# Performance work log

Hardware: AMD Instinct MI355X
Metric: run time of the kernel (lower is better)

## Reference

```python
import jax, jax.numpy as jnp
import numpy as np

D_MODEL, D_K, D_V, N_HEADS = 1024, 64, 64, 16


def setup_inputs() -> dict:
    key = jax.random.key(0)
    ks = jax.random.split(key, 8)
    B, S = 2, 2048
    s = 0.02
    return {
        "x": jax.random.normal(ks[0], (B, S, D_MODEL), dtype=jnp.float32),
        "Wq": jax.random.normal(ks[1], (D_MODEL, N_HEADS * D_K), dtype=jnp.float32) * s,
        "bq": jnp.zeros((N_HEADS * D_K,), dtype=jnp.float32),
        "Wk": jax.random.normal(ks[2], (D_MODEL, N_HEADS * D_K), dtype=jnp.float32) * s,
        "bk": jnp.zeros((N_HEADS * D_K,), dtype=jnp.float32),
        "Wv": jax.random.normal(ks[3], (D_MODEL, N_HEADS * D_V), dtype=jnp.float32) * s,
        "bv": jnp.zeros((N_HEADS * D_V,), dtype=jnp.float32),
        "Wo": jax.random.normal(ks[4], (N_HEADS * D_V, D_MODEL), dtype=jnp.float32) * s,
    }


def reference(x, Wq, bq, Wk, bk, Wv, bv, Wo):
    B, S, _ = x.shape
    split = lambda t, d: t.reshape(B, S, N_HEADS, d).transpose(0, 2, 1, 3)  # [B,H,S,d]
    Q = split(x @ Wq + bq, D_K)
    K = split(x @ Wk + bk, D_K)
    V = split(x @ Wv + bv, D_V)
    scores = jnp.einsum("bhqd,bhkd->bhqk", Q / jnp.sqrt(jnp.float32(D_K)), K)
    # causal mask: x + (1 - 1/tril) == 0 on allowed, -inf on disallowed
    causal = jnp.tril(jnp.ones((S, S), dtype=bool))
    scores = jnp.where(causal, scores, -jnp.inf)
    attn = jax.nn.softmax(scores, axis=-1)
    out = jnp.einsum("bhqk,bhkd->bhqd", attn, V)  # [B,H,S,d_v]
    out = out.transpose(0, 2, 1, 3).reshape(B, S, N_HEADS * D_V)
    return out @ Wo
```

## Files before the change

kernel.cpp:

```cpp
#include <hip/hip_runtime.h>
#include <hip/hip_bf16.h>
#include <hip/hip_fp16.h>
#include <cstdint>

#define DEVINL __device__ __forceinline__

typedef __attribute__((ext_vector_type(4))) float floatx4;
typedef __attribute__((ext_vector_type(8))) __bf16 bf16x8;
typedef __attribute__((ext_vector_type(4))) _Float16 half4;
typedef __attribute__((ext_vector_type(8))) _Float16 half8;
typedef __attribute__((ext_vector_type(4))) unsigned short u16x4;

DEVINL floatx4 mfma_16x16x32(bf16x8 a, bf16x8 b, floatx4 c) {
  return __builtin_amdgcn_mfma_f32_16x16x32_bf16(a, b, c, 0, 0, 0);
}
DEVINL floatx4 mfma_16x16x16_f16(half4 a, half4 b, floatx4 c) {
  return __builtin_amdgcn_mfma_f32_16x16x16f16(a, b, c, 0, 0, 0);
}

DEVINL void async_copy16(const void* g, void* l) {
  __builtin_amdgcn_global_load_lds(
      (__attribute__((address_space(1))) void*)(void*)g,
      (__attribute__((address_space(3))) void*)l, 16, 0, 0);
}

#define QSCALE 0.18033688011112042f

#define VS(d, s) \
  ((d) * 128 + (((((s) >> 3)) ^ ((d) & 7)) << 4) + ((s) & 7) * 2)

__global__ void prep(const float* __restrict__ x, const float* __restrict__ Wq,
                     const float* __restrict__ Wk, const float* __restrict__ Wv,
                     const float* __restrict__ Wo,
                     __hip_bfloat16* __restrict__ xb,
                     __hip_bfloat16* __restrict__ Wt,
                     __hip_bfloat16* __restrict__ Wot) {
  const int z = blockIdx.z;
  const int tx = threadIdx.x, ty = threadIdx.y;
  if (z == 4) {
    const int bi = blockIdx.y * 32 + blockIdx.x;
    const int tid = ty * 32 + tx;
    const int base = bi * 4096 + tid * 4;
#pragma unroll
    for (int j = 0; j < 4; ++j) {
      const int i = base + j * 1024;
      const float4 v = *(const float4*)&x[i];
      u16x4 pk;
      pk[0] = __builtin_bit_cast(unsigned short, __float2bfloat16(v.x));
      pk[1] = __builtin_bit_cast(unsigned short, __float2bfloat16(v.y));
      pk[2] = __builtin_bit_cast(unsigned short, __float2bfloat16(v.z));
      pk[3] = __builtin_bit_cast(unsigned short, __float2bfloat16(v.w));
      *(u16x4*)&xb[i] = pk;
    }
    return;
  }
  __shared__ float tile[32][33];
  const float* W = (z == 0) ? Wq : (z == 1) ? Wk : (z == 2) ? Wv : Wo;
  __hip_bfloat16* dst = (z < 3) ? (Wt + ((int64_t)z << 20)) : Wot;
  const int k0 = blockIdx.x * 32, n0 = blockIdx.y * 32;
#pragma unroll
  for (int i = 0; i < 32; i += 8)
    tile[ty + i][tx] = W[(int64_t)(k0 + ty + i) * 1024 + n0 + tx];
  __syncthreads();
#pragma unroll
  for (int i = 0; i < 32; i += 8)
    dst[(int64_t)(n0 + ty + i) * 1024 + k0 + tx] =
        __float2bfloat16(tile[tx][ty + i]);
}

template <int MODE, int TM, int TN, int OCC>
__global__ __launch_bounds__(256, OCC) void gemm_bt(
    const __hip_bfloat16* __restrict__ A, const __hip_bfloat16* __restrict__ Bt,
    int M, int N, int K, const float* __restrict__ bq,
    const float* __restrict__ bk, const float* __restrict__ bv,
    __hip_bfloat16* __restrict__ Qb, __hip_bfloat16* __restrict__ Kb,
    _Float16* __restrict__ Vt, float* __restrict__ outf) {
  constexpr int MI = TM / 32, NJ = TN / 32;
  __shared__ __align__(16) char As[TM * 128];
  __shared__ __align__(16) char Bs[TN * 128];
  const int tid = threadIdx.x;
  const int wave = tid >> 6, lane = tid & 63;
  const int quad = lane >> 4, l16 = lane & 15;
  const int bm = blockIdx.x * TM, bn = blockIdx.y * TN;
  const int wm = (wave >> 1) * (TM / 2), wn = (wave & 1) * (TN / 2);
  const int sw = l16 & 7;

  floatx4 acc[MI][NJ] = {};

  for (int k0 = 0; k0 < K; k0 += 64) {
#pragma unroll
    for (int i = 0; i < TM / 32; ++i) {
      const int p = tid + i * 256;
      const int r = p >> 3, cc = (p & 7) ^ (r & 7);
      async_copy16(A + (int64_t)(bm + r) * K + k0 + cc * 8, As + p * 16);
    }
#pragma unroll
    for (int i = 0; i < TN / 32; ++i) {
      const int p = tid + i * 256;
      const int r = p >> 3, cc = (p & 7) ^ (r & 7);
      async_copy16(Bt + (int64_t)(bn + r) * K + k0 + cc * 8, Bs + p * 16);
    }
    __syncthreads();
    bf16x8 af[MI][2], bfr[NJ][2];
#pragma unroll
    for (int i = 0; i < MI; ++i)
#pragma unroll
      for (int h = 0; h < 2; ++h)
        af[i][h] = *(const bf16x8*)(As + (wm + i * 16 + l16) * 128 +
                                    (((h * 4 + quad) ^ sw) << 4));
#pragma unroll
    for (int j = 0; j < NJ; ++j)
#pragma unroll
      for (int h = 0; h < 2; ++h)
        bfr[j][h] = *(const bf16x8*)(Bs + (wn + j * 16 + l16) * 128 +
                                     (((h * 4 + quad) ^ sw) << 4));
#pragma unroll
    for (int i = 0; i < MI; ++i)
#pragma unroll
      for (int j = 0; j < NJ; ++j)
#pragma unroll
        for (int h = 0; h < 2; ++h)
          acc[i][j] = mfma_16x16x32(af[i][h], bfr[j][h], acc[i][j]);
    __syncthreads();
  }

  if (MODE == 1) {
#pragma unroll
    for (int i = 0; i < MI; ++i)
#pragma unroll
      for (int j = 0; j < NJ; ++j) {
        const int n = bn + wn + j * 16 + l16;
#pragma unroll
        for (int r = 0; r < 4; ++r) {
          const int m = bm + wm + i * 16 + quad * 4 + r;
          outf[(int64_t)m * N + n] = acc[i][j][r];
        }
      }
  } else if (bn < 2048) {
#pragma unroll
    for (int i = 0; i < MI; ++i)
#pragma unroll
      for (int j = 0; j < NJ; ++j) {
        const int n = bn + wn + j * 16 + l16;
        const int which = n >> 10, nn = n & 1023;
        const int h = nn >> 6, d = nn & 63;
        const float* bias = (which == 0) ? bq : bk;
#pragma unroll
        for (int r = 0; r < 4; ++r) {
          const int m = bm + wm + i * 16 + quad * 4 + r;
          const int b = m >> 11, s = m & 2047;
          float v = acc[i][j][r] + bias[nn];
          if (which == 0) v *= QSCALE;
          ((which == 0) ? Qb : Kb)[((int64_t)(b * 16 + h) * 2048 + s) * 64 + d] =
              __float2bfloat16(v);
        }
      }
  } else {
    char* scr = (wave & 1) ? Bs : As;
    const int h = ((bn + wn) & 1023) >> 6;
    const int bb = (bm + wm) >> 11;
    const int sbase = (bm + wm) & 2047;
    _Float16* dstV = Vt + (int64_t)(bb * 16 + h) * 64 * 2048;
#pragma unroll
    for (int phase = 0; phase < 2; ++phase) {
      __syncthreads();
      if ((wave >> 1) == phase) {
#pragma unroll
        for (int i = 0; i < 4; ++i)
#pragma unroll
          for (int j = 0; j < 4; ++j) {
            const int d = j * 16 + l16;
#pragma unroll
            for (int r = 0; r < 4; ++r) {
              const int s = i * 16 + quad * 4 + r;
              *(_Float16*)(scr + VS(d, s)) =
                  (_Float16)(acc[i][j][r] + bv[((bn + wn) & 1023) + d]);
            }
          }
      }
      __syncthreads();
      if ((wave >> 1) == phase) {
#pragma unroll
        for (int it = 0; it < 8; ++it) {
          const int idx = lane + it * 64;
          const int d = idx >> 3, sc = idx & 7;
          const half8 vv =
              *(const half8*)(scr + d * 128 + ((sc ^ (d & 7)) << 4));
          *(half8*)(dstV + (int64_t)d * 2048 + sbase + sc * 8) = vv;
        }
      }
    }
  }
}

__global__ __launch_bounds__(256, 2) void attn_kernel(
    const __hip_bfloat16* __restrict__ Qb, const __hip_bfloat16* __restrict__ Kb,
    const _Float16* __restrict__ Vt, __hip_bfloat16* __restrict__ Ab) {
  __shared__ __align__(16) char smem[32768];
  const int tid = threadIdx.x;
  const int wave = tid >> 6, lane = tid & 63;
  const int quad = lane >> 4, l16 = lane & 15;
  const int pr = (int)(blockIdx.x >> 5);
  const int bh = blockIdx.x & 31;
  const int cH = 31 - pr, cL = pr;
  const int qH = cH * 64 + wave * 16;
  const int qL = cL * 64 + wave * 16;
  const int ktmax = cH;

  const __hip_bfloat16* Qh = Qb + (int64_t)bh * 2048 * 64;
  const __hip_bfloat16* Kh = Kb + (int64_t)bh * 2048 * 64;
  const _Float16* Vh = Vt + (int64_t)bh * 64 * 2048;

  bf16x8 qfH[2], qfL[2];
#pragma unroll
  for (int h = 0; h < 2; ++h) {
    qfH[h] = *(const bf16x8*)&Qh[(int64_t)(qH + l16) * 64 + h * 32 + quad * 8];
    qfL[h] = *(const bf16x8*)&Qh[(int64_t)(qL + l16) * 64 + h * 32 + quad * 8];
  }

  floatx4 oH[4] = {}, oL[4] = {};
  float lsH = 0.f, lsL = 0.f;

  auto stage = [&](int buf, int k0s) {
#pragma unroll
    for (int i = 0; i < 2; ++i) {
      const int p = tid + i * 256;
      const int r = p >> 3, cc = (p & 7) ^ (r & 7);
      async_copy16(Kh + (int64_t)(k0s + r) * 64 + cc * 8,
                   smem + buf * 8192 + p * 16);
      async_copy16(Vh + (int64_t)r * 2048 + k0s + cc * 8,
                   smem + 16384 + buf * 8192 + p * 16);
    }
  };

  stage(0, 0);
  for (int kt = 0; kt <= ktmax; ++kt) {
    const int k0 = kt * 64;
    const int cur = kt & 1;
    __syncthreads();
    if (kt < ktmax) stage(cur ^ 1, k0 + 64);

    const char* kb = smem + cur * 8192;
    const char* vb = smem + 16384 + cur * 8192;
    const int sw = l16 & 7;
    const bool doL = (kt <= cL);

    bf16x8 kfr[4][2];
#pragma unroll
    for (int kk = 0; kk < 4; ++kk)
#pragma unroll
      for (int h = 0; h < 2; ++h)
        kfr[kk][h] = *(const bf16x8*)(kb + (kk * 16 + l16) * 128 +
                                      (((h * 4 + quad) ^ sw) << 4));
    half4 vfr[4][4];
#pragma unroll
    for (int dt = 0; dt < 4; ++dt)
#pragma unroll
      for (int kk = 0; kk < 4; ++kk)
        vfr[dt][kk] = *(const half4*)(vb + (dt * 16 + l16) * 128 +
                                      (((kk * 2 + (quad >> 1)) ^ sw) << 4) +
                                      (quad & 1) * 8);

    floatx4 stH[4], stL[4];
    __builtin_amdgcn_s_setprio(1);
#pragma unroll
    for (int kk = 0; kk < 4; ++kk) {
      floatx4 z = {};
      z = mfma_16x16x32(kfr[kk][0], qfH[0], z);
      stH[kk] = mfma_16x16x32(kfr[kk][1], qfH[1], z);
    }
    if (doL) {
#pragma unroll
      for (int kk = 0; kk < 4; ++kk) {
        floatx4 z = {};
        z = mfma_16x16x32(kfr[kk][0], qfL[0], z);
        stL[kk] = mfma_16x16x32(kfr[kk][1], qfL[1], z);
      }
    }
    __builtin_amdgcn_s_setprio(0);

    {
      const bool masked = (kt == cH);
      half4 pf[4];
#pragma unroll
      for (int kk = 0; kk < 4; ++kk) {
#pragma unroll
        for (int r = 0; r < 4; ++r) {
          const int key = k0 + kk * 16 + quad * 4 + r;
          float p = __builtin_amdgcn_exp2f(stH[kk][r]);
          if (masked && key > qH + l16) p = 0.f;
          lsH += p;
          pf[kk][r] = (_Float16)p;
        }
      }
      __builtin_amdgcn_s_setprio(1);
#pragma unroll
      for (int dt = 0; dt < 4; ++dt)
#pragma unroll
        for (int kk = 0; kk < 4; ++kk)
          oH[dt] = mfma_16x16x16_f16(vfr[dt][kk], pf[kk], oH[dt]);
      __builtin_amdgcn_s_setprio(0);
    }
    if (doL) {
      const bool masked = (kt == cL);
      half4 pf[4];
#pragma unroll
      for (int kk = 0; kk < 4; ++kk) {
#pragma unroll
        for (int r = 0; r < 4; ++r) {
          const int key = k0 + kk * 16 + quad * 4 + r;
          float p = __builtin_amdgcn_exp2f(stL[kk][r]);
          if (masked && key > qL + l16) p = 0.f;
          lsL += p;
          pf[kk][r] = (_Float16)p;
        }
      }
      __builtin_amdgcn_s_setprio(1);
#pragma unroll
      for (int dt = 0; dt < 4; ++dt)
#pragma unroll
        for (int kk = 0; kk < 4; ++kk)
          oL[dt] = mfma_16x16x16_f16(vfr[dt][kk], pf[kk], oL[dt]);
      __builtin_amdgcn_s_setprio(0);
    }
  }

  lsH += __shfl_xor(lsH, 16, 64);
  lsH += __shfl_xor(lsH, 32, 64);
  lsL += __shfl_xor(lsL, 16, 64);
  lsL += __shfl_xor(lsL, 32, 64);
  const float invH = 1.0f / lsH;
  const float invL = 1.0f / lsL;

  const int b = bh >> 4, h = bh & 15;
#pragma unroll
  for (int dt = 0; dt < 4; ++dt) {
    u16x4 packH, packL;
#pragma unroll
    for (int r = 0; r < 4; ++r) {
      packH[r] = __builtin_bit_cast(unsigned short,
                                    __float2bfloat16(oH[dt][r] * invH));
      packL[r] = __builtin_bit_cast(unsigned short,
                                    __float2bfloat16(oL[dt][r] * invL));
    }
    *(u16x4*)&Ab[(int64_t)(b * 2048 + qH + l16) * 1024 + h * 64 + dt * 16 +
                 quad * 4] = packH;
    *(u16x4*)&Ab[(int64_t)(b * 2048 + qL + l16) * 1024 + h * 64 + dt * 16 +
                 quad * 4] = packL;
  }
}

extern "C" void kernel_launch(void* const* d_in, const int* in_sizes, int n_in,
                              void* d_out, int out_size, void* d_ws,
                              size_t ws_size, hipStream_t stream) {
  const float* x = (const float*)d_in[0];
  const float* Wq = (const float*)d_in[1];
  const float* bq = (const float*)d_in[2];
  const float* Wk = (const float*)d_in[3];
  const float* bk = (const float*)d_in[4];
  const float* Wv = (const float*)d_in[5];
  const float* bv = (const float*)d_in[6];
  const float* Wo = (const float*)d_in[7];
  float* out = (float*)d_out;

  char* ws = (char*)d_ws;
  __hip_bfloat16* xb = (__hip_bfloat16*)(ws);
  __hip_bfloat16* Wt = (__hip_bfloat16*)(ws + (8ll << 20));
  __hip_bfloat16* Wot = (__hip_bfloat16*)(ws + (14ll << 20));
  __hip_bfloat16* Qb = (__hip_bfloat16*)(ws + (16ll << 20));
  __hip_bfloat16* Kb = (__hip_bfloat16*)(ws + (24ll << 20));
  _Float16* Vt = (_Float16*)(ws + (32ll << 20));
  __hip_bfloat16* Ab = xb;

  prep<<<dim3(32, 32, 5), dim3(32, 8), 0, stream>>>(x, Wq, Wk, Wv, Wo, xb, Wt,
                                                    Wot);
  gemm_bt<0, 128, 128, 3><<<dim3(32, 24), 256, 0, stream>>>(
      xb, Wt, 4096, 3072, 1024, bq, bk, bv, Qb, Kb, Vt, nullptr);
  attn_kernel<<<dim3(512), 256, 0, stream>>>(Qb, Kb, Vt, Ab);
  gemm_bt<1, 128, 64, 2><<<dim3(32, 16), 256, 0, stream>>>(
      Ab, Wot, 4096, 1024, 1024, nullptr, nullptr, nullptr, nullptr, nullptr,
      nullptr, out);
}
```

Baseline: 165.5 us.

## Add dedicated 256x256 double-buffered QKV projection GEMM kernel

Result: slower. 172.3 us (+4.1%).

```diff
diff --git a/kernel.cpp b/kernel.cpp
--- a/kernel.cpp
+++ b/kernel.cpp
@@ -68,13 +68,135 @@
         __float2bfloat16(tile[tx][ty + i]);
 }
 
+__global__ __launch_bounds__(512, 2) void gemm_qkv(
+    const __hip_bfloat16* __restrict__ A, const __hip_bfloat16* __restrict__ Bt,
+    const float* __restrict__ bq, const float* __restrict__ bk,
+    const float* __restrict__ bv, __hip_bfloat16* __restrict__ Qb,
+    __hip_bfloat16* __restrict__ Kb, _Float16* __restrict__ Vt) {
+  __shared__ __align__(16) char smem[131072];
+  const int tid = threadIdx.x;
+  const int wave = tid >> 6, lane = tid & 63;
+  const int quad = lane >> 4, l16 = lane & 15;
+  const int wr = wave >> 2, wc = wave & 3;
+  const int bm = blockIdx.x * 256, bn = blockIdx.y * 256;
+  const int K = 1024;
+
+  floatx4 acc[8][4] = {};
+
+  auto stage_tile = [&](int buf, int kt) {
+    char* base = smem + buf * 65536;
+    const int k0 = kt * 64;
+#pragma unroll
+    for (int i = 0; i < 4; ++i) {
+      const int p = tid + i * 512;
+      const int r = p >> 3, cc = (p & 7) ^ (r & 7);
+      async_copy16(A + (int64_t)(bm + r) * K + k0 + cc * 8, base + p * 16);
+    }
+#pragma unroll
+    for (int i = 0; i < 4; ++i) {
+      const int p = tid + i * 512;
+      const int r = p >> 3, cc = (p & 7) ^ (r & 7);
+      async_copy16(Bt + (int64_t)(bn + r) * K + k0 + cc * 8,
+                   base + 32768 + p * 16);
+    }
+  };
+
+  stage_tile(0, 0);
+  for (int t = 0; t < 16; ++t) {
+    __syncthreads();
+    if (t + 1 < 16) stage_tile((t + 1) & 1, t + 1);
+
+    const char* ab = smem + (t & 1) * 65536;
+    const char* bb = ab + 32768;
+#pragma unroll
+    for (int ph = 0; ph < 4; ++ph) {
+      const int m0 = (ph >> 1) * 4, n0 = (ph & 1) * 2;
+      bf16x8 af[4][2], bf[2][2];
+#pragma unroll
+      for (int i = 0; i < 4; ++i) {
+        const int rr = wr * 128 + (m0 + i) * 16 + l16;
+#pragma unroll
+        for (int h = 0; h < 2; ++h)
+          af[i][h] = *(const bf16x8*)(ab + rr * 128 +
+                                      (((h * 4 + quad) ^ (rr & 7)) << 4));
+      }
+#pragma unroll
+      for (int j = 0; j < 2; ++j) {
+        const int rr = wc * 64 + (n0 + j) * 16 + l16;
+#pragma unroll
+        for (int h = 0; h < 2; ++h)
+          bf[j][h] = *(const bf16x8*)(bb + rr * 128 +
+                                      (((h * 4 + quad) ^ (rr & 7)) << 4));
+      }
+      __builtin_amdgcn_s_setprio(1);
+#pragma unroll
+      for (int i = 0; i < 4; ++i)
+#pragma unroll
+        for (int j = 0; j < 2; ++j)
+#pragma unroll
+          for (int h = 0; h < 2; ++h)
+            acc[m0 + i][n0 + j] =
+                mfma_16x16x32(af[i][h], bf[j][h], acc[m0 + i][n0 + j]);
+      __builtin_amdgcn_s_setprio(0);
+    }
+  }
+
+  const int colbase = bn + wc * 64;
+  if (bn < 2048) {
+    const int which = colbase >> 10;
+    const float* bias = (which == 0) ? bq : bk;
+    __hip_bfloat16* dst = (which == 0) ? Qb : Kb;
+#pragma unroll
+    for (int mi = 0; mi < 8; ++mi)
+#pragma unroll
+      for (int nj = 0; nj < 4; ++nj) {
+        const int n = colbase + nj * 16 + l16;
+        const int nn = n & 1023, hh = nn >> 6, d = nn & 63;
+#pragma unroll
+        for (int r = 0; r < 4; ++r) {
+          const int m = bm + wr * 128 + mi * 16 + quad * 4 + r;
+          const int b = m >> 11, s = m & 2047;
+          float v = acc[mi][nj][r] + bias[nn];
+          if (which == 0) v *= QSCALE;
+          dst[((int64_t)(b * 16 + hh) * 2048 + s) * 64 + d] =
+              __float2bfloat16(v);
+        }
+      }
+  } else {
+    __syncthreads();
+    char* scr = smem + wave * 16384;
+    const int hh = (colbase & 1023) >> 6;
+    const int mrow = bm + wr * 128;
+    const int bb2 = mrow >> 11, sbase = mrow & 2047;
+#pragma unroll
+    for (int mi = 0; mi < 8; ++mi)
+#pragma unroll
+      for (int nj = 0; nj < 4; ++nj) {
+        const int d = nj * 16 + l16;
+#pragma unroll
+        for (int r = 0; r < 4; ++r) {
+          const int s = mi * 16 + quad * 4 + r;
+          *(_Float16*)(scr + d * 256 + ((((s >> 3) ^ (d & 15))) << 4) +
+                       (s & 7) * 2) =
+              (_Float16)(acc[mi][nj][r] + bv[(colbase & 1023) + d]);
+        }
+      }
+    asm volatile("s_waitcnt lgkmcnt(0)" ::: "memory");
+    _Float16* dstV = Vt + (int64_t)(bb2 * 16 + hh) * 64 * 2048;
+#pragma unroll
+    for (int it = 0; it < 16; ++it) {
+      const int idx = lane + it * 64;
+      const int d = idx >> 4, sc = idx & 15;
+      const half8 vv = *(const half8*)(scr + d * 256 + ((sc ^ (d & 15)) << 4));
+      *(half8*)(dstV + (int64_t)d * 2048 + sbase + sc * 8) = vv;
+    }
+  }
+}
+
 template <int MODE, int TM, int TN, int OCC>
 __global__ __launch_bounds__(256, OCC) void gemm_bt(
     const __hip_bfloat16* __restrict__ A, const __hip_bfloat16* __restrict__ Bt,
-    int M, int N, int K, const float* __restrict__ bq,
-    const float* __restrict__ bk, const float* __restrict__ bv,
-    __hip_bfloat16* __restrict__ Qb, __hip_bfloat16* __restrict__ Kb,
-    _Float16* __restrict__ Vt, float* __restrict__ outf) {
+    int M, int N, int K, float* __restrict__ outf) {
   constexpr int MI = TM / 32, NJ = TN / 32;
   __shared__ __align__(16) char As[TM * 128];
   __shared__ __align__(16) char Bs[TN * 128];
@@ -124,73 +246,17 @@
     __syncthreads();
   }
 
-  if (MODE == 1) {
-#pragma unroll
-    for (int i = 0; i < MI; ++i)
-#pragma unroll
-      for (int j = 0; j < NJ; ++j) {
-        const int n = bn + wn + j * 16 + l16;
-#pragma unroll
-        for (int r = 0; r < 4; ++r) {
-          const int m = bm + wm + i * 16 + quad * 4 + r;
-          outf[(int64_t)m * N + n] = acc[i][j][r];
-        }
-      }
-  } else if (bn < 2048) {
-#pragma unroll
-    for (int i = 0; i < MI; ++i)
-#pragma unroll
-      for (int j = 0; j < NJ; ++j) {
-        const int n = bn + wn + j * 16 + l16;
-        const int which = n >> 10, nn = n & 1023;
-        const int h = nn >> 6, d = nn & 63;
-        const float* bias = (which == 0) ? bq : bk;
-#pragma unroll
-        for (int r = 0; r < 4; ++r) {
-          const int m = bm + wm + i * 16 + quad * 4 + r;
-          const int b = m >> 11, s = m & 2047;
-          float v = acc[i][j][r] + bias[nn];
-          if (which == 0) v *= QSCALE;
-          ((which == 0) ? Qb : Kb)[((int64_t)(b * 16 + h) * 2048 + s) * 64 + d] =
-              __float2bfloat16(v);
-        }
-      }
-  } else {
-    char* scr = (wave & 1) ? Bs : As;
-    const int h = ((bn + wn) & 1023) >> 6;
-    const int bb = (bm + wm) >> 11;
-    const int sbase = (bm + wm) & 2047;
-    _Float16* dstV = Vt + (int64_t)(bb * 16 + h) * 64 * 2048;
-#pragma unroll
-    for (int phase = 0; phase < 2; ++phase) {
-      __syncthreads();
-      if ((wave >> 1) == phase) {
-#pragma unroll
-        for (int i = 0; i < 4; ++i)
-#pragma unroll
-          for (int j = 0; j < 4; ++j) {
-            const int d = j * 16 + l16;
-#pragma unroll
-            for (int r = 0; r < 4; ++r) {
-              const int s = i * 16 + quad * 4 + r;
-              *(_Float16*)(scr + VS(d, s)) =
-                  (_Float16)(acc[i][j][r] + bv[((bn + wn) & 1023) + d]);
-            }
-          }
-      }
-      __syncthreads();
-      if ((wave >> 1) == phase) {
-#pragma unroll
-        for (int it = 0; it < 8; ++it) {
-          const int idx = lane + it * 64;
-          const int d = idx >> 3, sc = idx & 7;
-          const half8 vv =
-              *(const half8*)(scr + d * 128 + ((sc ^ (d & 7)) << 4));
-          *(half8*)(dstV + (int64_t)d * 2048 + sbase + sc * 8) = vv;
-        }
-      }
-    }
-  }
+#pragma unroll
+  for (int i = 0; i < MI; ++i)
+#pragma unroll
+    for (int j = 0; j < NJ; ++j) {
+      const int n = bn + wn + j * 16 + l16;
+#pragma unroll
+      for (int r = 0; r < 4; ++r) {
+        const int m = bm + wm + i * 16 + quad * 4 + r;
+        outf[(int64_t)m * N + n] = acc[i][j][r];
+      }
+    }
 }
 
 __global__ __launch_bounds__(256, 2) void attn_kernel(
@@ -374,10 +440,8 @@
 
   prep<<<dim3(32, 32, 5), dim3(32, 8), 0, stream>>>(x, Wq, Wk, Wv, Wo, xb, Wt,
                                                     Wot);
-  gemm_bt<0, 128, 128, 3><<<dim3(32, 24), 256, 0, stream>>>(
-      xb, Wt, 4096, 3072, 1024, bq, bk, bv, Qb, Kb, Vt, nullptr);
+  gemm_qkv<<<dim3(16, 12), 512, 0, stream>>>(xb, Wt, bq, bk, bv, Qb, Kb, Vt);
   attn_kernel<<<dim3(512), 256, 0, stream>>>(Qb, Kb, Vt, Ab);
   gemm_bt<1, 128, 64, 2><<<dim3(32, 16), 256, 0, stream>>>(
-      Ab, Wot, 4096, 1024, 1024, nullptr, nullptr, nullptr, nullptr, nullptr,
-      nullptr, out);
-}
+      Ab, Wot, 4096, 1024, 1024, out);
+}
```
